# Performance work log

Hardware: AMD Instinct MI355X
Metric: run time of the kernel (lower is better)

## Reference

```python
import jax, jax.numpy as jnp
import numpy as np

BATCH = 4096
NNZ = 32
VOCAB = 1_000_000
DIM = 64


def setup_inputs() -> dict:
    key = jax.random.key(0)
    k1, k2, k3, k4 = jax.random.split(key, 4)
    idx = jax.random.randint(k1, (BATCH, NNZ), 0, VOCAB, dtype=jnp.int32)
    vals = jax.random.uniform(k2, (BATCH, NNZ), dtype=jnp.float32)
    kernel = jax.random.normal(k3, (VOCAB, DIM), dtype=jnp.float32)
    bias = jax.random.normal(k4, (DIM,), dtype=jnp.float32)
    return {"idx": idx, "vals": vals, "kernel": kernel, "bias": bias}


def reference(idx, vals, kernel, bias):
    # Sparse [B, V] x dense [V, D] matmul == weighted gather-sum (embedding bag)
    gathered = kernel[idx]                      # [B, nnz, D] irregular gather
    out = jnp.einsum("bn,bnd->bd", vals, gathered) + bias  # [B, D]
    return out
```

## Files before the change

### kernel.cpp

```cpp
#include <hip/hip_runtime.h>
#include <hip/hip_bf16.h>


#define B_BATCH 4096
#define NNZ 32
#define DIM 64

__global__ __launch_bounds__(256) void sparse_embed_kernel(
    const int* __restrict__ idx,
    const float* __restrict__ vals,
    const float* __restrict__ kern,
    const float* __restrict__ bias,
    float* __restrict__ out)
{
    const int lane = threadIdx.x & 63;
    int row = (blockIdx.x << 2) + (threadIdx.x >> 6);
    row = __builtin_amdgcn_readfirstlane(row);

    const int*   irow = idx  + row * NNZ;
    const float* vrow = vals + row * NNZ;

    int   ids[NNZ];
    float vs[NNZ];
    #pragma unroll
    for (int n = 0; n < NNZ; ++n) {
        ids[n] = irow[n];
        vs[n]  = vrow[n];
    }

    float acc = bias[lane];

    #pragma unroll
    for (int n = 0; n < NNZ; ++n) {
        const float k = kern[(size_t)ids[n] * DIM + lane];
        acc = fmaf(vs[n], k, acc);
    }

    out[row * DIM + lane] = acc;
}

extern "C" void kernel_launch(void* const* d_in, const int* in_sizes, int n_in,
                              void* d_out, int out_size, void* d_ws, size_t ws_size,
                              hipStream_t stream) {
    const int*   idx  = (const int*)  d_in[0];
    const float* vals = (const float*)d_in[1];
    const float* kern = (const float*)d_in[2];
    const float* bias = (const float*)d_in[3];
    float* out = (float*)d_out;

    const int threads = 256;
    const int blocks  = B_BATCH / 4;

    sparse_embed_kernel<<<blocks, threads, 0, stream>>>(idx, vals, kern, bias, out);
}
```

Measured before the change: 297.2 us.

## Gather embedding rows with float4 loads across four nnz groups per wave

```diff
diff --git a/kernel.cpp b/kernel.cpp
--- a/kernel.cpp
+++ b/kernel.cpp
@@ -14,29 +14,43 @@
     float* __restrict__ out)
 {
     const int lane = threadIdx.x & 63;
+    const int g    = lane >> 4;
+    const int s    = lane & 15;
     int row = (blockIdx.x << 2) + (threadIdx.x >> 6);
     row = __builtin_amdgcn_readfirstlane(row);
 
-    const int*   irow = idx  + row * NNZ;
-    const float* vrow = vals + row * NNZ;
+    const int   allid  = idx [row * NNZ + (lane & 31)];
+    const float allval = vals[row * NNZ + (lane & 31)];
 
-    int   ids[NNZ];
-    float vs[NNZ];
+    float4 acc = make_float4(0.f, 0.f, 0.f, 0.f);
+
     #pragma unroll
-    for (int n = 0; n < NNZ; ++n) {
-        ids[n] = irow[n];
-        vs[n]  = vrow[n];
+    for (int n = 0; n < NNZ; n += 4) {
+        const int   src = n + g;
+        const int   id  = __shfl(allid,  src);
+        const float v   = __shfl(allval, src);
+        const float4 k  = *reinterpret_cast<const float4*>(
+            kern + (size_t)id * DIM + s * 4);
+        acc.x = fmaf(v, k.x, acc.x);
+        acc.y = fmaf(v, k.y, acc.y);
+        acc.z = fmaf(v, k.z, acc.z);
+        acc.w = fmaf(v, k.w, acc.w);
     }
 
-    float acc = bias[lane];
+    acc.x += __shfl_xor(acc.x, 16); acc.y += __shfl_xor(acc.y, 16);
+    acc.z += __shfl_xor(acc.z, 16); acc.w += __shfl_xor(acc.w, 16);
+    acc.x += __shfl_xor(acc.x, 32); acc.y += __shfl_xor(acc.y, 32);
+    acc.z += __shfl_xor(acc.z, 32); acc.w += __shfl_xor(acc.w, 32);
 
-    #pragma unroll
-    for (int n = 0; n < NNZ; ++n) {
-        const float k = kern[(size_t)ids[n] * DIM + lane];
-        acc = fmaf(vs[n], k, acc);
+    if (lane < 16) {
+        const float4 b4 = *reinterpret_cast<const float4*>(bias + s * 4);
+        float4 r;
+        r.x = acc.x + b4.x;
+        r.y = acc.y + b4.y;
+        r.z = acc.z + b4.z;
+        r.w = acc.w + b4.w;
+        *reinterpret_cast<float4*>(out + (size_t)row * DIM + s * 4) = r;
     }
-
-    out[row * DIM + lane] = acc;
 }
 
 extern "C" void kernel_launch(void* const* d_in, const int* in_sizes, int n_in,
```

After: 297.8 us. Within noise of the previous version (+0.2%).
